# Performance work log

Measured on AMD Instinct MI355X. Metric: run time of the kernel, lower is better.

The kernel has to match this reference:

```python
import jax, jax.numpy as jnp
import numpy as np

H, C, L = 4, 64, 3          # heads, out_channels, conv layers
N, E, B = 20000, 320000, 32 # nodes, edges, graphs
HD = 64                     # hidden_dim


def setup_inputs() -> dict:
    key = jax.random.key(0)
    ks = jax.random.split(key, 24)
    x = jax.random.normal(ks[0], (N, 3), jnp.float32)
    src = jax.random.randint(ks[1], (E,), 0, N)
    dst = jax.random.randint(ks[2], (E,), 0, N)
    dst = jnp.where(dst == src, (dst + 1) % N, dst)  # no pre-existing self loops
    edge_index = jnp.stack([src, dst])
    edge_attr = jax.random.normal(ks[3], (E, 4), jnp.float32)
    u = jax.random.normal(ks[4], (B, 10), jnp.float32)
    batch = jnp.sort(jax.random.randint(ks[5], (N,), 0, B))
    p = lambda k, s: jax.random.normal(k, s, jnp.float32) * 0.1
    return {
        'x': x, 'edge_index': edge_index, 'edge_attr': edge_attr, 'u': u, 'batch': batch,
        'node_W': p(ks[6], (3, HD)), 'node_b': p(ks[7], (HD,)),
        'eemb_W': p(ks[8], (4, HD)), 'eemb_b': p(ks[9], (HD,)),
        'lin_W': p(ks[10], (L, HD, H * C)),
        'att_src': p(ks[11], (L, H, C)), 'att_dst': p(ks[12], (L, H, C)),
        'lin_eW': p(ks[13], (L, HD, H * C)), 'att_e': p(ks[14], (L, H, C)),
        'conv_b': p(ks[15], (L, C)),
        'gW': p(ks[16], (10, HD)), 'gb': p(ks[17], (HD,)),
        'f1W': p(ks[18], (2 * HD, HD)), 'f1b': p(ks[19], (HD,)),
        'f2W': p(ks[20], (HD, 2)), 'f2b': p(ks[21], (2,)),
    }


def _gat_layer(x, src, dst, ea, W, a_src, a_dst, We, a_e, b):
    # PyG GATConv(hidden, hidden, edge_dim=hidden, heads=4, concat=False), eval mode
    n = x.shape[0]
    # add self loops; self-loop edge_attr = mean of incoming edge_attr (fill_value='mean')
    deg = jax.ops.segment_sum(jnp.ones_like(dst, dtype=x.dtype), dst, num_segments=n)
    ea_self = jax.ops.segment_sum(ea, dst, num_segments=n) / jnp.maximum(deg, 1.0)[:, None]
    loop = jnp.arange(n)
    src2 = jnp.concatenate([src, loop])
    dst2 = jnp.concatenate([dst, loop])
    ea2 = jnp.concatenate([ea, ea_self], axis=0)
    xp = (x @ W).reshape(n, H, C)                       # [N,H,C]
    a_s = jnp.einsum('nhc,hc->nh', xp, a_src)           # [N,H]
    a_d = jnp.einsum('nhc,hc->nh', xp, a_dst)
    ee = (ea2 @ We).reshape(-1, H, C)                   # [E2,H,C]
    a_ed = jnp.einsum('ehc,hc->eh', ee, a_e)
    alpha = jax.nn.leaky_relu(a_s[src2] + a_d[dst2] + a_ed, 0.2)  # [E2,H]
    # segment softmax over destination nodes (stable)
    m = jax.ops.segment_max(alpha, dst2, num_segments=n)
    ex = jnp.exp(alpha - m[dst2])
    den = jax.ops.segment_sum(ex, dst2, num_segments=n)
    att = ex / den[dst2]
    out = jax.ops.segment_sum(xp[src2] * att[..., None], dst2, num_segments=n)  # [N,H,C]
    return out.mean(axis=1) + b  # concat=False -> mean over heads


def reference(x, edge_index, edge_attr, u, batch, node_W, node_b, eemb_W, eemb_b,
              lin_W, att_src, att_dst, lin_eW, att_e, conv_b, gW, gb, f1W, f1b, f2W, f2b):
    src, dst = edge_index[0], edge_index[1]
    h = jax.nn.relu(x @ node_W + node_b)
    ea = jax.nn.relu(edge_attr @ eemb_W + eemb_b)
    for i in range(L):
        h = jax.nn.relu(_gat_layer(h, src, dst, ea, lin_W[i], att_src[i], att_dst[i],
                                   lin_eW[i], att_e[i], conv_b[i]))
    # global mean pool over graphs
    cnt = jax.ops.segment_sum(jnp.ones((h.shape[0],), h.dtype), batch, num_segments=B)
    pooled = jax.ops.segment_sum(h, batch, num_segments=B) / jnp.maximum(cnt, 1.0)[:, None]
    ug = jax.nn.relu(u @ gW + gb)
    z = jnp.concatenate([pooled, ug], axis=1)
    z = jax.nn.relu(z @ f1W + f1b)
    return z @ f2W + f2b
```

## Files before the change

### kernel.cpp

```cpp
#include <hip/hip_runtime.h>
#include <hip/hip_bf16.h>

#define HD 64

typedef unsigned short u16;

__device__ __forceinline__ float lrelu(float x) { return x > 0.f ? x : 0.2f * x; }
__device__ __forceinline__ int clampi(int v, int maxv) {
    return v < 0 ? 0 : (v >= maxv ? maxv - 1 : v);
}
__device__ __forceinline__ float bf2f(u16 u) {
    return __uint_as_float(((unsigned int)u) << 16);
}
__device__ __forceinline__ u16 f2bf(float f) {
    unsigned int u = __float_as_uint(f);
    unsigned int lsb = (u >> 16) & 1u;
    u += 0x7fffu + lsb;
    return (u16)(u >> 16);
}

__global__ void k_init(const float* __restrict__ x, const float* __restrict__ W,
                       const float* __restrict__ b, float* __restrict__ h,
                       const float* __restrict__ lin_W, const float* __restrict__ att_src,
                       const float* __restrict__ att_dst, float* __restrict__ wsd,
                       int* deg, int* cursor, float* pooled, int N, int B) {
    int i = blockIdx.x * blockDim.x + threadIdx.x;
    if (i < N) { deg[i] = 0; cursor[i] = 0; }
    if (i < B * HD) pooled[i] = 0.f;
    if (i < 3 * 512) {
        int l = i >> 9, r = i & 511;
        int idx = r >> 6, d = r & 63;
        int hh = idx >> 1, sel = idx & 1;
        const float* att = (sel ? att_dst : att_src) + l * 256 + hh * 64;
        const float* Wrow = lin_W + (size_t)l * HD * 256 + d * 256 + hh * 64;
        float acc = 0.f;
        for (int c = 0; c < 64; c++) acc = fmaf(Wrow[c], att[c], acc);
        wsd[(l << 9) + (idx << 6) + d] = acc;
    }
    if (i < N * HD) {
        int n = i >> 6, c = i & 63;
        float acc = b[c];
        acc = fmaf(x[n * 3 + 0], W[0 * HD + c], acc);
        acc = fmaf(x[n * 3 + 1], W[1 * HD + c], acc);
        acc = fmaf(x[n * 3 + 2], W[2 * HD + c], acc);
        h[i] = fmaxf(acc, 0.f);
    }
}

__global__ void k_att(const float* __restrict__ h, const float* __restrict__ wsdl,
                      float* __restrict__ a_s, float* __restrict__ a_d, int N) {
    int i = blockIdx.x * blockDim.x + threadIdx.x;
    if (i >= N * 8) return;
    int n = i >> 3, idx = i & 7;
    const float* hr = h + (size_t)n * HD;
    const float* wp = wsdl + (idx << 6);
    float a = 0.f;
    for (int d = 0; d < HD; d += 4) {
        float4 hv = *(const float4*)(hr + d);
        float4 wv = *(const float4*)(wp + d);
        a = fmaf(hv.x, wv.x, a); a = fmaf(hv.y, wv.y, a);
        a = fmaf(hv.z, wv.z, a); a = fmaf(hv.w, wv.w, a);
    }
    int hd = idx >> 1, sel = idx & 1;
    if (sel) a_d[n * 4 + hd] = a;
    else     a_s[n * 4 + hd] = a;
}

__global__ void k_deg(const int* __restrict__ dst, int* __restrict__ deg, int E, int N) {
    int e = blockIdx.x * blockDim.x + threadIdx.x;
    if (e < E) atomicAdd(&deg[clampi(dst[e], N)], 1);
}

__global__ void k_scan1(const int* __restrict__ deg, int* __restrict__ tmp,
                        int* __restrict__ bsum, int N) {
    __shared__ int s[256];
    int tid = threadIdx.x;
    int i = blockIdx.x * 256 + tid;
    int v = (i < N) ? deg[i] : 0;
    s[tid] = v;
    __syncthreads();
    for (int off = 1; off < 256; off <<= 1) {
        int t = (tid >= off) ? s[tid - off] : 0;
        __syncthreads();
        s[tid] += t;
        __syncthreads();
    }
    if (i < N) tmp[i] = s[tid];
    if (tid == 255) bsum[blockIdx.x] = s[255];
}
__global__ void k_scan23(const int* __restrict__ tmp, const int* __restrict__ bsum,
                         int* __restrict__ row_ptr, int N) {
    __shared__ int s_off;
    int t = threadIdx.x;
    if (t < 64) {
        int cnt = blockIdx.x;
        int v = 0;
        for (int base = 0; base < cnt; base += 64)
            if (base + t < cnt) v += bsum[base + t];
        #pragma unroll
        for (int o = 32; o > 0; o >>= 1) v += __shfl_xor(v, o);
        if (t == 0) s_off = v;
    }
    __syncthreads();
    int i = blockIdx.x * 256 + t;
    if (i == 0) row_ptr[0] = 0;
    if (i < N) row_ptr[i + 1] = tmp[i] + s_off;
}

__global__ void k_csr(const int* __restrict__ src, const int* __restrict__ dst,
                      const int* __restrict__ row_ptr, int* __restrict__ cursor,
                      int2* __restrict__ csr_se, int E, int N) {
    int e = blockIdx.x * blockDim.x + threadIdx.x;
    if (e >= E) return;
    int d = clampi(dst[e], N);
    int pos = row_ptr[d] + atomicAdd(&cursor[d], 1);
    if (pos < E) csr_se[pos] = make_int2(clampi(src[e], N), e);
}

__global__ __launch_bounds__(256) void k_ee(
    const float* __restrict__ edge_attr, const float* __restrict__ eW,
    const float* __restrict__ eB, const float* __restrict__ lin_eW,
    const float* __restrict__ att_e, const int2* __restrict__ csr_se,
    float* __restrict__ aed, int E, int N) {
    __shared__ float s_ew[256];
    __shared__ float s_eb[64];
    __shared__ float s_wred[768];
    size_t P4 = (size_t)(E + N) * 4;
    int t = threadIdx.x;
    s_ew[t] = eW[t];
    if (t < 64) s_eb[t] = eB[t];
    for (int idx = t; idx < 768; idx += 256) {
        int l = idx >> 8, hd = idx & 255, hh = hd >> 6, d = hd & 63;
        const float* We = lin_eW + (size_t)l * HD * 256;
        const float* ae = att_e + (size_t)l * 256;
        float acc = 0.f;
        for (int c = 0; c < 64; c++)
            acc = fmaf(We[d * 256 + hh * 64 + c], ae[hh * 64 + c], acc);
        s_wred[idx] = acc;
    }
    __syncthreads();
    int j0 = (blockIdx.x * 256 + t) * 4;
    if (j0 >= E) return;
    float4 a[4];
    int nv = 0;
    #pragma unroll
    for (int q = 0; q < 4; q++) {
        int j = j0 + q;
        if (j < E) {
            a[q] = *(const float4*)(edge_attr + (size_t)csr_se[j].y * 4);
            nv = q + 1;
        } else {
            a[q] = make_float4(0.f, 0.f, 0.f, 0.f);
        }
    }
    float acc[4][12];
    #pragma unroll
    for (int q = 0; q < 4; q++)
        #pragma unroll
        for (int m = 0; m < 12; m++) acc[q][m] = 0.f;
    for (int k = 0; k < HD; k++) {
        float e0 = s_ew[k], e1 = s_ew[64 + k], e2 = s_ew[128 + k], e3 = s_ew[192 + k];
        float eb = s_eb[k];
        float w[12];
        #pragma unroll
        for (int m = 0; m < 12; m++)
            w[m] = s_wred[(m >> 2) * 256 + (m & 3) * 64 + k];
        #pragma unroll
        for (int q = 0; q < 4; q++) {
            float v = fmaf(a[q].x, e0, fmaf(a[q].y, e1,
                      fmaf(a[q].z, e2, fmaf(a[q].w, e3, eb))));
            v = fmaxf(v, 0.f);
            #pragma unroll
            for (int m = 0; m < 12; m++) acc[q][m] = fmaf(v, w[m], acc[q][m]);
        }
    }
    #pragma unroll
    for (int q = 0; q < 4; q++) {
        if (q >= nv) break;
        #pragma unroll
        for (int l = 0; l < 3; l++) {
            *(float4*)(aed + l * P4 + (size_t)(j0 + q) * 4) =
                make_float4(acc[q][l * 4 + 0], acc[q][l * 4 + 1],
                            acc[q][l * 4 + 2], acc[q][l * 4 + 3]);
        }
    }
}

__global__ void k_selfed(const int* __restrict__ row_ptr, float* __restrict__ aed,
                         int E, int N) {
    int n = blockIdx.x * blockDim.x + threadIdx.x;
    if (n >= N) return;
    size_t P4 = (size_t)(E + N) * 4;
    int r0 = row_ptr[n], r1 = row_ptr[n + 1];
    float acc[12];
    #pragma unroll
    for (int m = 0; m < 12; m++) acc[m] = 0.f;
    for (int j = r0; j < r1; j++) {
        #pragma unroll
        for (int l = 0; l < 3; l++) {
            float4 v = *(const float4*)(aed + l * P4 + (size_t)j * 4);
            acc[l * 4 + 0] += v.x; acc[l * 4 + 1] += v.y;
            acc[l * 4 + 2] += v.z; acc[l * 4 + 3] += v.w;
        }
    }
    float inv = 1.f / fmaxf((float)(r1 - r0), 1.f);
    #pragma unroll
    for (int l = 0; l < 3; l++) {
        *(float4*)(aed + l * P4 + (size_t)(E + n) * 4) =
            make_float4(acc[l * 4 + 0] * inv, acc[l * 4 + 1] * inv,
                        acc[l * 4 + 2] * inv, acc[l * 4 + 3] * inv);
    }
}

__global__ __launch_bounds__(256) void k_gat(
    const float* __restrict__ h, const float* __restrict__ a_s,
    const float* __restrict__ a_d, const float* __restrict__ aedl,
    const int* __restrict__ row_ptr, const int2* __restrict__ csr_se,
    u16* __restrict__ z, int N, int E) {
    int wave = threadIdx.x >> 6, lane = threadIdx.x & 63;
    int n = blockIdx.x * 4 + wave;
    if (n >= N) return;
    int g = lane >> 4, p = lane & 15;
    int r0 = row_ptr[n], r1 = row_ptr[n + 1];
    float4 ad4 = *(const float4*)(a_d + (size_t)n * 4);
    float a00 = 0.f, a01 = 0.f, a02 = 0.f, a03 = 0.f;
    float a10 = 0.f, a11 = 0.f, a12 = 0.f, a13 = 0.f;
    float a20 = 0.f, a21 = 0.f, a22 = 0.f, a23 = 0.f;
    float a30 = 0.f, a31 = 0.f, a32 = 0.f, a33 = 0.f;
    float d0 = 0.f, d1 = 0.f, d2 = 0.f, d3 = 0.f;
    if (g == 0) {
        float4 as4 = *(const float4*)(a_s + (size_t)n * 4);
        float4 p4 = *(const float4*)(aedl + (size_t)(E + n) * 4);
        float w0 = __expf(lrelu(as4.x + ad4.x + p4.x));
        float w1 = __expf(lrelu(as4.y + ad4.y + p4.y));
        float w2 = __expf(lrelu(as4.z + ad4.z + p4.z));
        float w3 = __expf(lrelu(as4.w + ad4.w + p4.w));
        float4 hv = *(const float4*)(h + (size_t)n * HD + p * 4);
        d0 += w0; d1 += w1; d2 += w2; d3 += w3;
        a00 = fmaf(w0, hv.x, a00); a01 = fmaf(w0, hv.y, a01);
        a02 = fmaf(w0, hv.z, a02); a03 = fmaf(w0, hv.w, a03);
        a10 = fmaf(w1, hv.x, a10); a11 = fmaf(w1, hv.y, a11);
        a12 = fmaf(w1, hv.z, a12); a13 = fmaf(w1, hv.w, a13);
        a20 = fmaf(w2, hv.x, a20); a21 = fmaf(w2, hv.y, a21);
        a22 = fmaf(w2, hv.z, a22); a23 = fmaf(w2, hv.w, a23);
        a30 = fmaf(w3, hv.x, a30); a31 = fmaf(w3, hv.y, a31);
        a32 = fmaf(w3, hv.z, a32); a33 = fmaf(w3, hv.w, a33);
    }
    int j = r0 + g;
    int2 se = (j < r1) ? csr_se[j] : make_int2(0, 0);
    for (; j < r1; j += 4) {
        int jn = j + 4;
        int2 se_n = (jn < r1) ? csr_se[jn] : make_int2(0, 0);
        int s = se.x;
        float4 as4 = *(const float4*)(a_s + (size_t)s * 4);
        float4 p4 = *(const float4*)(aedl + (size_t)j * 4);
        float w0 = __expf(lrelu(as4.x + ad4.x + p4.x));
        float w1 = __expf(lrelu(as4.y + ad4.y + p4.y));
        float w2 = __expf(lrelu(as4.z + ad4.z + p4.z));
        float w3 = __expf(lrelu(as4.w + ad4.w + p4.w));
        float4 hv = *(const float4*)(h + (size_t)s * HD + p * 4);
        d0 += w0; d1 += w1; d2 += w2; d3 += w3;
        a00 = fmaf(w0, hv.x, a00); a01 = fmaf(w0, hv.y, a01);
        a02 = fmaf(w0, hv.z, a02); a03 = fmaf(w0, hv.w, a03);
        a10 = fmaf(w1, hv.x, a10); a11 = fmaf(w1, hv.y, a11);
        a12 = fmaf(w1, hv.z, a12); a13 = fmaf(w1, hv.w, a13);
        a20 = fmaf(w2, hv.x, a20); a21 = fmaf(w2, hv.y, a21);
        a22 = fmaf(w2, hv.z, a22); a23 = fmaf(w2, hv.w, a23);
        a30 = fmaf(w3, hv.x, a30); a31 = fmaf(w3, hv.y, a31);
        a32 = fmaf(w3, hv.z, a32); a33 = fmaf(w3, hv.w, a33);
        se = se_n;
    }
    d0 += __shfl_xor(d0, 16); d0 += __shfl_xor(d0, 32);
    d1 += __shfl_xor(d1, 16); d1 += __shfl_xor(d1, 32);
    d2 += __shfl_xor(d2, 16); d2 += __shfl_xor(d2, 32);
    d3 += __shfl_xor(d3, 16); d3 += __shfl_xor(d3, 32);
    a00 += __shfl_xor(a00, 16); a00 += __shfl_xor(a00, 32);
    a01 += __shfl_xor(a01, 16); a01 += __shfl_xor(a01, 32);
    a02 += __shfl_xor(a02, 16); a02 += __shfl_xor(a02, 32);
    a03 += __shfl_xor(a03, 16); a03 += __shfl_xor(a03, 32);
    a10 += __shfl_xor(a10, 16); a10 += __shfl_xor(a10, 32);
    a11 += __shfl_xor(a11, 16); a11 += __shfl_xor(a11, 32);
    a12 += __shfl_xor(a12, 16); a12 += __shfl_xor(a12, 32);
    a13 += __shfl_xor(a13, 16); a13 += __shfl_xor(a13, 32);
    a20 += __shfl_xor(a20, 16); a20 += __shfl_xor(a20, 32);
    a21 += __shfl_xor(a21, 16); a21 += __shfl_xor(a21, 32);
    a22 += __shfl_xor(a22, 16); a22 += __shfl_xor(a22, 32);
    a23 += __shfl_xor(a23, 16); a23 += __shfl_xor(a23, 32);
    a30 += __shfl_xor(a30, 16); a30 += __shfl_xor(a30, 32);
    a31 += __shfl_xor(a31, 16); a31 += __shfl_xor(a31, 32);
    a32 += __shfl_xor(a32, 16); a32 += __shfl_xor(a32, 32);
    a33 += __shfl_xor(a33, 16); a33 += __shfl_xor(a33, 32);
    if (lane < 16) {
        float i0 = 1.f / d0, i1 = 1.f / d1, i2 = 1.f / d2, i3 = 1.f / d3;
        u16* zr = z + (size_t)n * 256 + p * 4;
        *(ushort4*)(zr)       = make_ushort4(f2bf(a00 * i0), f2bf(a01 * i0),
                                             f2bf(a02 * i0), f2bf(a03 * i0));
        *(ushort4*)(zr + 64)  = make_ushort4(f2bf(a10 * i1), f2bf(a11 * i1),
                                             f2bf(a12 * i1), f2bf(a13 * i1));
        *(ushort4*)(zr + 128) = make_ushort4(f2bf(a20 * i2), f2bf(a21 * i2),
                                             f2bf(a22 * i2), f2bf(a23 * i2));
        *(ushort4*)(zr + 192) = make_ushort4(f2bf(a30 * i3), f2bf(a31 * i3),
                                             f2bf(a32 * i3), f2bf(a33 * i3));
    }
}

#define PNB 8
__global__ __launch_bounds__(256) void k_post(
    const u16* __restrict__ z, const float* __restrict__ W,
    const float* __restrict__ convb, const float* __restrict__ wsdn,
    float* __restrict__ h_out, float* __restrict__ a_s, float* __restrict__ a_d, int N) {
    __shared__ float sred[4 * PNB * 64];
    __shared__ float hnew[PNB * 64];
    int t = threadIdx.x;
    int c = t & 63, kq = t >> 6;
    int n0 = blockIdx.x * PNB;
    int nlim = N - n0;
    const u16* zp = z + (size_t)n0 * 256;
    float acc[PNB];
    #pragma unroll
    for (int m = 0; m < PNB; m++) acc[m] = 0.f;
    for (int kk = 0; kk < 16; kk++) {
        int k4 = kq * 64 + kk * 4;
        int base = (k4 >> 6) * 64 + c;
        float wv0 = W[((k4 & 63) + 0) * 256 + base];
        float wv1 = W[((k4 & 63) + 1) * 256 + base];
        float wv2 = W[((k4 & 63) + 2) * 256 + base];
        float wv3 = W[((k4 & 63) + 3) * 256 + base];
        #pragma unroll
        for (int m = 0; m < PNB; m++) {
            int mm = (m < nlim) ? m : 0;
            ushort4 zz = *(const ushort4*)(zp + (size_t)mm * 256 + k4);
            acc[m] = fmaf(bf2f(zz.x), wv0, acc[m]);
            acc[m] = fmaf(bf2f(zz.y), wv1, acc[m]);
            acc[m] = fmaf(bf2f(zz.z), wv2, acc[m]);
            acc[m] = fmaf(bf2f(zz.w), wv3, acc[m]);
        }
    }
    #pragma unroll
    for (int m = 0; m < PNB; m++) sred[(kq * PNB + m) * 64 + c] = acc[m];
    __syncthreads();
    if (kq == 0) {
        #pragma unroll
        for (int m = 0; m < PNB; m++) {
            float v = sred[m * 64 + c] + sred[(PNB + m) * 64 + c] +
                      sred[(2 * PNB + m) * 64 + c] + sred[(3 * PNB + m) * 64 + c];
            v = fmaxf(0.25f * v + convb[c], 0.f);
            hnew[m * 64 + c] = v;
            if (m < nlim) h_out[(size_t)(n0 + m) * HD + c] = v;
        }
    }
    __syncthreads();
    if (t < PNB * 8) {
        int m = t >> 3, idx = t & 7;
        if (m < nlim) {
            const float* wp = wsdn + (idx << 6);
            float a = 0.f;
            for (int d = 0; d < HD; d++) a = fmaf(hnew[m * 64 + d], wp[d], a);
            int hd = idx >> 1, sel = idx & 1;
            if (sel) a_d[(size_t)(n0 + m) * 4 + hd] = a;
            else     a_s[(size_t)(n0 + m) * 4 + hd] = a;
        }
    }
}

#define PCHUNK 8
__global__ void k_pool(const float* __restrict__ h, const int* __restrict__ batch,
                       float* __restrict__ pooled, int N, int B) {
    int b = blockIdx.x / PCHUNK, q = blockIdx.x % PCHUNK;
    __shared__ int sb[2];
    __shared__ float sred[256];
    int t = threadIdx.x;
    if (t == 0 || t == 64) {
        int target = b + (t ? 1 : 0);
        int lo = 0, hi = N;
        while (lo < hi) {
            int m = (lo + hi) >> 1;
            if (batch[m] < target) lo = m + 1; else hi = m;
        }
        sb[t ? 1 : 0] = lo;
    }
    __syncthreads();
    int start = sb[0], end = sb[1];
    int len = end - start;
    int c0 = start + (int)(((long long)len * q) / PCHUNK);
    int c1 = start + (int)(((long long)len * (q + 1)) / PCHUNK);
    int c = t & 63, r = t >> 6;
    float acc = 0.f;
    for (int nidx = c0 + r; nidx < c1; nidx += 4)
        acc += h[(size_t)nidx * HD + c];
    sred[t] = acc;
    __syncthreads();
    if (t < 64) {
        float v = sred[t] + sred[64 + t] + sred[128 + t] + sred[192 + t];
        if (v != 0.f) atomicAdd(&pooled[b * HD + c], v);
    }
}

__global__ void k_mlp(const float* __restrict__ u, const float* __restrict__ gW,
                      const float* __restrict__ gb, const float* __restrict__ pooled,
                      const int* __restrict__ batch, const float* __restrict__ f1W,
                      const float* __restrict__ f1b, const float* __restrict__ f2W,
                      const float* __restrict__ f2b, float* __restrict__ out,
                      int N, int B) {
    __shared__ float z[2 * HD];
    __shared__ float z1s[HD];
    __shared__ int sb[2];
    int b = blockIdx.x, t = threadIdx.x;
    if (t < 2) {
        int target = b + t;
        int lo = 0, hi = N;
        while (lo < hi) {
            int m = (lo + hi) >> 1;
            if (batch[m] < target) lo = m + 1; else hi = m;
        }
        sb[t] = lo;
    }
    float acc = gb[t];
    for (int k = 0; k < 10; k++) acc = fmaf(u[b * 10 + k], gW[k * HD + t], acc);
    z[HD + t] = fmaxf(acc, 0.f);
    __syncthreads();
    float invc = 1.f / fmaxf((float)(sb[1] - sb[0]), 1.f);
    z[t] = pooled[b * HD + t] * invc;
    __syncthreads();
    float a1 = f1b[t];
    for (int k = 0; k < 2 * HD; k++) a1 = fmaf(z[k], f1W[k * HD + t], a1);
    z1s[t] = fmaxf(a1, 0.f);
    __syncthreads();
    if (t < 2) {
        float o = f2b[t];
        for (int k = 0; k < HD; k++) o = fmaf(z1s[k], f2W[k * 2 + t], o);
        out[b * 2 + t] = o;
    }
}

extern "C" void kernel_launch(void* const* d_in, const int* in_sizes, int n_in,
                              void* d_out, int out_size, void* d_ws, size_t ws_size,
                              hipStream_t stream) {
    const float* x         = (const float*)d_in[0];
    const int*   ei        = (const int*)d_in[1];
    const float* edge_attr = (const float*)d_in[2];
    const float* u         = (const float*)d_in[3];
    const int*   batch     = (const int*)d_in[4];
    const float* node_W    = (const float*)d_in[5];
    const float* node_b    = (const float*)d_in[6];
    const float* eemb_W    = (const float*)d_in[7];
    const float* eemb_b    = (const float*)d_in[8];
    const float* lin_W     = (const float*)d_in[9];
    const float* att_src   = (const float*)d_in[10];
    const float* att_dst   = (const float*)d_in[11];
    const float* lin_eW    = (const float*)d_in[12];
    const float* att_e     = (const float*)d_in[13];
    const float* conv_b    = (const float*)d_in[14];
    const float* gW        = (const float*)d_in[15];
    const float* gb        = (const float*)d_in[16];
    const float* f1W       = (const float*)d_in[17];
    const float* f1b       = (const float*)d_in[18];
    const float* f2W       = (const float*)d_in[19];
    const float* f2b       = (const float*)d_in[20];

    const int N = in_sizes[0] / 3;
    const int E = in_sizes[2] / 4;
    const int B = in_sizes[3] / 10;
    const int* src = ei;
    const int* dst = ei + E;
    const int NB = (N + 255) / 256;
    const size_t P4 = (size_t)(E + N) * 4;

    float* wsf = (float*)d_ws;
    float* h       = wsf;              wsf += (size_t)N * HD;
    float* a_s     = wsf;              wsf += (size_t)N * 4;
    float* a_d     = wsf;              wsf += (size_t)N * 4;
    float* aed     = wsf;              wsf += 3 * P4;
    float* pooled  = wsf;              wsf += (size_t)B * HD;
    float* wsd     = wsf;              wsf += 3 * 512;
    u16* zbuf = (u16*)wsf;             wsf += (size_t)N * 128;
    int* wsi = (int*)wsf;
    int2* csr_se = (int2*)wsi;         wsi += 2 * (size_t)E;
    int* deg     = wsi;                wsi += N;
    int* row_ptr = wsi;                wsi += N + 1;
    int* cursor  = wsi;                wsi += N;
    int* tmp     = wsi;                wsi += N;
    int* bsum    = wsi;                wsi += NB + 1;

    k_init<<<(N * HD + 255) / 256, 256, 0, stream>>>(x, node_W, node_b, h,
                                                     lin_W, att_src, att_dst, wsd,
                                                     deg, cursor, pooled, N, B);
    k_deg<<<(E + 255) / 256, 256, 0, stream>>>(dst, deg, E, N);
    k_scan1<<<NB, 256, 0, stream>>>(deg, tmp, bsum, N);
    k_scan23<<<NB, 256, 0, stream>>>(tmp, bsum, row_ptr, N);
    k_csr<<<(E + 255) / 256, 256, 0, stream>>>(src, dst, row_ptr, cursor,
                                               csr_se, E, N);
    k_ee<<<(E + 1023) / 1024, 256, 0, stream>>>(edge_attr, eemb_W, eemb_b, lin_eW, att_e,
                                                csr_se, aed, E, N);
    k_selfed<<<NB, 256, 0, stream>>>(row_ptr, aed, E, N);
    k_att<<<(N * 8 + 255) / 256, 256, 0, stream>>>(h, wsd, a_s, a_d, N);
    for (int i = 0; i < 3; i++) {
        k_gat<<<(N + 3) / 4, 256, 0, stream>>>(h, a_s, a_d, aed + (size_t)i * P4,
                                               row_ptr, csr_se, zbuf, N, E);
        const float* wsdn = wsd + (size_t)(i < 2 ? i + 1 : 2) * 512;
        k_post<<<(N + PNB - 1) / PNB, 256, 0, stream>>>(zbuf,
                                                        lin_W + (size_t)i * HD * 256,
                                                        conv_b + (size_t)i * HD,
                                                        wsdn, h, a_s, a_d, N);
    }
    k_pool<<<B * PCHUNK, 256, 0, stream>>>(h, batch, pooled, N, B);
    k_mlp<<<B, 64, 0, stream>>>(u, gW, gb, pooled, batch, f1W, f1b, f2W, f2b,
                                (float*)d_out, N, B);
}
```

Before: 447.0 us.

## Store GAT aggregate in fp32, restructure post-projection, split attention logits kernel

The per-node aggregated buffer z is now written in fp32 instead of bf16, which removes the rounding conversions but doubles that buffer's memory traffic. k_post is restructured so each wave handles 8 nodes over the full 256-wide reduction, which drops the shared-memory cross-wave reduction and both block barriers. The fused attention-logit computation is moved out of k_post into a separate k_att launch per layer. This trades extra launches and more bandwidth for simpler, barrier-free projection kernels.

```diff
diff --git a/kernel.cpp b/kernel.cpp
--- a/kernel.cpp
+++ b/kernel.cpp
@@ -8,15 +8,6 @@
 __device__ __forceinline__ float lrelu(float x) { return x > 0.f ? x : 0.2f * x; }
 __device__ __forceinline__ int clampi(int v, int maxv) {
     return v < 0 ? 0 : (v >= maxv ? maxv - 1 : v);
-}
-__device__ __forceinline__ float bf2f(u16 u) {
-    return __uint_as_float(((unsigned int)u) << 16);
-}
-__device__ __forceinline__ u16 f2bf(float f) {
-    unsigned int u = __float_as_uint(f);
-    unsigned int lsb = (u >> 16) & 1u;
-    u += 0x7fffu + lsb;
-    return (u16)(u >> 16);
 }
 
 __global__ void k_init(const float* __restrict__ x, const float* __restrict__ W,
@@ -216,7 +207,7 @@
     const float* __restrict__ h, const float* __restrict__ a_s,
     const float* __restrict__ a_d, const float* __restrict__ aedl,
     const int* __restrict__ row_ptr, const int2* __restrict__ csr_se,
-    u16* __restrict__ z, int N, int E) {
+    float* __restrict__ z, int N, int E) {
     int wave = threadIdx.x >> 6, lane = threadIdx.x & 63;
     int n = blockIdx.x * 4 + wave;
     if (n >= N) return;
@@ -292,74 +283,49 @@
     a33 += __shfl_xor(a33, 16); a33 += __shfl_xor(a33, 32);
     if (lane < 16) {
         float i0 = 1.f / d0, i1 = 1.f / d1, i2 = 1.f / d2, i3 = 1.f / d3;
-        u16* zr = z + (size_t)n * 256 + p * 4;
-        *(ushort4*)(zr)       = make_ushort4(f2bf(a00 * i0), f2bf(a01 * i0),
-                                             f2bf(a02 * i0), f2bf(a03 * i0));
-        *(ushort4*)(zr + 64)  = make_ushort4(f2bf(a10 * i1), f2bf(a11 * i1),
-                                             f2bf(a12 * i1), f2bf(a13 * i1));
-        *(ushort4*)(zr + 128) = make_ushort4(f2bf(a20 * i2), f2bf(a21 * i2),
-                                             f2bf(a22 * i2), f2bf(a23 * i2));
-        *(ushort4*)(zr + 192) = make_ushort4(f2bf(a30 * i3), f2bf(a31 * i3),
-                                             f2bf(a32 * i3), f2bf(a33 * i3));
-    }
-}
-
-#define PNB 8
+        float* zr = z + (size_t)n * 256 + p * 4;
+        *(float4*)(zr)       = make_float4(a00 * i0, a01 * i0, a02 * i0, a03 * i0);
+        *(float4*)(zr + 64)  = make_float4(a10 * i1, a11 * i1, a12 * i1, a13 * i1);
+        *(float4*)(zr + 128) = make_float4(a20 * i2, a21 * i2, a22 * i2, a23 * i2);
+        *(float4*)(zr + 192) = make_float4(a30 * i3, a31 * i3, a32 * i3, a33 * i3);
+    }
+}
+
+#define PNB 32
 __global__ __launch_bounds__(256) void k_post(
-    const u16* __restrict__ z, const float* __restrict__ W,
-    const float* __restrict__ convb, const float* __restrict__ wsdn,
-    float* __restrict__ h_out, float* __restrict__ a_s, float* __restrict__ a_d, int N) {
-    __shared__ float sred[4 * PNB * 64];
-    __shared__ float hnew[PNB * 64];
+    const float* __restrict__ z, const float* __restrict__ W,
+    const float* __restrict__ convb, float* __restrict__ h_out, int N) {
     int t = threadIdx.x;
-    int c = t & 63, kq = t >> 6;
-    int n0 = blockIdx.x * PNB;
+    int c = t & 63, ng = t >> 6;
+    int n0 = blockIdx.x * PNB + ng * 8;
     int nlim = N - n0;
-    const u16* zp = z + (size_t)n0 * 256;
-    float acc[PNB];
-    #pragma unroll
-    for (int m = 0; m < PNB; m++) acc[m] = 0.f;
-    for (int kk = 0; kk < 16; kk++) {
-        int k4 = kq * 64 + kk * 4;
+    if (nlim <= 0) return;
+    const float* zp = z + (size_t)n0 * 256;
+    float acc[8];
+    #pragma unroll
+    for (int m = 0; m < 8; m++) acc[m] = 0.f;
+    for (int k4 = 0; k4 < 256; k4 += 4) {
         int base = (k4 >> 6) * 64 + c;
-        float wv0 = W[((k4 & 63) + 0) * 256 + base];
-        float wv1 = W[((k4 & 63) + 1) * 256 + base];
-        float wv2 = W[((k4 & 63) + 2) * 256 + base];
-        float wv3 = W[((k4 & 63) + 3) * 256 + base];
-        #pragma unroll
-        for (int m = 0; m < PNB; m++) {
+        float w0 = W[((k4 & 63) + 0) * 256 + base];
+        float w1 = W[((k4 & 63) + 1) * 256 + base];
+        float w2 = W[((k4 & 63) + 2) * 256 + base];
+        float w3 = W[((k4 & 63) + 3) * 256 + base];
+        #pragma unroll
+        for (int m = 0; m < 8; m++) {
             int mm = (m < nlim) ? m : 0;
-            ushort4 zz = *(const ushort4*)(zp + (size_t)mm * 256 + k4);
-            acc[m] = fmaf(bf2f(zz.x), wv0, acc[m]);
-            acc[m] = fmaf(bf2f(zz.y), wv1, acc[m]);
-            acc[m] = fmaf(bf2f(zz.z), wv2, acc[m]);
-            acc[m] = fmaf(bf2f(zz.w), wv3, acc[m]);
-        }
-    }
-    #pragma unroll
-    for (int m = 0; m < PNB; m++) sred[(kq * PNB + m) * 64 + c] = acc[m];
-    __syncthreads();
-    if (kq == 0) {
-        #pragma unroll
-        for (int m = 0; m < PNB; m++) {
-            float v = sred[m * 64 + c] + sred[(PNB + m) * 64 + c] +
-                      sred[(2 * PNB + m) * 64 + c] + sred[(3 * PNB + m) * 64 + c];
-            v = fmaxf(0.25f * v + convb[c], 0.f);
-            hnew[m * 64 + c] = v;
-            if (m < nlim) h_out[(size_t)(n0 + m) * HD + c] = v;
-        }
-    }
-    __syncthreads();
-    if (t < PNB * 8) {
-        int m = t >> 3, idx = t & 7;
-        if (m < nlim) {
-            const float* wp = wsdn + (idx << 6);
-            float a = 0.f;
-            for (int d = 0; d < HD; d++) a = fmaf(hnew[m * 64 + d], wp[d], a);
-            int hd = idx >> 1, sel = idx & 1;
-            if (sel) a_d[(size_t)(n0 + m) * 4 + hd] = a;
-            else     a_s[(size_t)(n0 + m) * 4 + hd] = a;
-        }
+            float4 zz = *(const float4*)(zp + (size_t)mm * 256 + k4);
+            acc[m] = fmaf(zz.x, w0, acc[m]);
+            acc[m] = fmaf(zz.y, w1, acc[m]);
+            acc[m] = fmaf(zz.z, w2, acc[m]);
+            acc[m] = fmaf(zz.w, w3, acc[m]);
+        }
+    }
+    float cb = convb[c];
+    #pragma unroll
+    for (int m = 0; m < 8; m++) {
+        int nn = n0 + m;
+        if (m < nlim)
+            h_out[(size_t)nn * HD + c] = fmaxf(0.25f * acc[m] + cb, 0.f);
     }
 }
 
@@ -473,7 +439,7 @@
     float* aed     = wsf;              wsf += 3 * P4;
     float* pooled  = wsf;              wsf += (size_t)B * HD;
     float* wsd     = wsf;              wsf += 3 * 512;
-    u16* zbuf = (u16*)wsf;             wsf += (size_t)N * 128;
+    float* zbuf    = wsf;              wsf += (size_t)N * 256;
     int* wsi = (int*)wsf;
     int2* csr_se = (int2*)wsi;         wsi += 2 * (size_t)E;
     int* deg     = wsi;                wsi += N;
@@ -497,11 +463,12 @@
     for (int i = 0; i < 3; i++) {
         k_gat<<<(N + 3) / 4, 256, 0, stream>>>(h, a_s, a_d, aed + (size_t)i * P4,
                                                row_ptr, csr_se, zbuf, N, E);
-        const float* wsdn = wsd + (size_t)(i < 2 ? i + 1 : 2) * 512;
         k_post<<<(N + PNB - 1) / PNB, 256, 0, stream>>>(zbuf,
                                                         lin_W + (size_t)i * HD * 256,
-                                                        conv_b + (size_t)i * HD,
-                                                        wsdn, h, a_s, a_d, N);
+                                                        conv_b + (size_t)i * HD, h, N);
+        if (i < 2)
+            k_att<<<(N * 8 + 255) / 256, 256, 0, stream>>>(h, wsd + (size_t)(i + 1) * 512,
+                                                           a_s, a_d, N);
     }
     k_pool<<<B * PCHUNK, 256, 0, stream>>>(h, batch, pooled, N, B);
     k_mlp<<<B, 64, 0, stream>>>(u, gW, gb, pooled, batch, f1W, f1b, f2W, f2b,
```

Measured after the change: 473.4 us. 5.9% more time.
